# Kernel tuning notes

Hardware: AMD Instinct MI355X
Metric: run time of the kernel (lower is better)

The kernel has to match this reference:

```python
import jax, jax.numpy as jnp
import numpy as np

BS, T = 128, 256
N_AGENTS, STATE_DIM, EMBED_DIM, HYPERNET_EMBED = 32, 512, 64, 256


def setup_inputs() -> dict:
    key = jax.random.key(0)
    ks = jax.random.split(key, 16)
    s = 0.02  # param init scale
    return {
        "agent_qs": jax.random.normal(ks[0], (BS, T, N_AGENTS), jnp.float32),
        "states": jax.random.normal(ks[1], (BS, T, STATE_DIM), jnp.float32),
        "w1_0": jax.random.normal(ks[2], (HYPERNET_EMBED, STATE_DIM), jnp.float32) * s,
        "b1_0": jax.random.normal(ks[3], (HYPERNET_EMBED,), jnp.float32) * s,
        "w1_2": jax.random.normal(ks[4], (EMBED_DIM * N_AGENTS, HYPERNET_EMBED), jnp.float32) * s,
        "b1_2": jax.random.normal(ks[5], (EMBED_DIM * N_AGENTS,), jnp.float32) * s,
        "wf_0": jax.random.normal(ks[6], (HYPERNET_EMBED, STATE_DIM), jnp.float32) * s,
        "bf_0": jax.random.normal(ks[7], (HYPERNET_EMBED,), jnp.float32) * s,
        "wf_2": jax.random.normal(ks[8], (EMBED_DIM, HYPERNET_EMBED), jnp.float32) * s,
        "bf_2": jax.random.normal(ks[9], (EMBED_DIM,), jnp.float32) * s,
        "hb_w": jax.random.normal(ks[10], (EMBED_DIM, STATE_DIM), jnp.float32) * s,
        "hb_b": jax.random.normal(ks[11], (EMBED_DIM,), jnp.float32) * s,
        "v0_w": jax.random.normal(ks[12], (EMBED_DIM, STATE_DIM), jnp.float32) * s,
        "v0_b": jax.random.normal(ks[13], (EMBED_DIM,), jnp.float32) * s,
        "v2_w": jax.random.normal(ks[14], (1, EMBED_DIM), jnp.float32) * s,
        "v2_b": jax.random.normal(ks[15], (1,), jnp.float32) * s,
    }


def reference(agent_qs, states, w1_0, b1_0, w1_2, b1_2, wf_0, bf_0, wf_2, bf_2,
              hb_w, hb_b, v0_w, v0_b, v2_w, v2_b):
    bs = agent_qs.shape[0]
    s = states.reshape(-1, STATE_DIM)          # [B, S]
    q = agent_qs.reshape(-1, 1, N_AGENTS)       # [B, 1, A]
    # hypernet-generated first-layer weights (positive via abs)
    h1 = jax.nn.relu(s @ w1_0.T + b1_0)
    w1 = jnp.abs(h1 @ w1_2.T + b1_2).reshape(-1, N_AGENTS, EMBED_DIM)  # [B, A, E]
    b1 = (s @ hb_w.T + hb_b).reshape(-1, 1, EMBED_DIM)                 # [B, 1, E]
    hidden = jax.nn.elu(jnp.einsum('bia,bae->bie', q, w1) + b1)        # [B, 1, E]
    # hypernet-generated final weights
    hf = jax.nn.relu(s @ wf_0.T + bf_0)
    w_final = jnp.abs(hf @ wf_2.T + bf_2).reshape(-1, EMBED_DIM, 1)    # [B, E, 1]
    v = (jax.nn.relu(s @ v0_w.T + v0_b) @ v2_w.T + v2_b).reshape(-1, 1, 1)
    y = jnp.einsum('bie,beo->bio', hidden, w_final) + v                # [B, 1, 1]
    return y.reshape(bs, -1, 1)
```

## Files before the change

### kernel.cpp

```cpp
#include <hip/hip_runtime.h>


#define SDIM 512
#define HD   256
#define EDIM 64
#define NAG  32

typedef short short8v __attribute__((ext_vector_type(8)));
typedef short short4v __attribute__((ext_vector_type(4)));
typedef float f32x4  __attribute__((ext_vector_type(4)));

__device__ __forceinline__ unsigned short f2bf(float f) {
  unsigned int u = __float_as_uint(f);
  unsigned int r = (u + 0x7FFFu + ((u >> 16) & 1u)) >> 16;
  return (unsigned short)r;
}
__device__ __forceinline__ float bf2f(unsigned short u) {
  return __uint_as_float(((unsigned int)u) << 16);
}
__device__ __forceinline__ short4v cvt4(float4 a) {
  short4v r;
  r[0] = (short)f2bf(a.x); r[1] = (short)f2bf(a.y);
  r[2] = (short)f2bf(a.z); r[3] = (short)f2bf(a.w);
  return r;
}

__global__ void qmix_convert(const float* __restrict__ w1_0, const float* __restrict__ wf_0,
                             const float* __restrict__ hb_w, const float* __restrict__ v0_w,
                             const float* __restrict__ w1_2, const float* __restrict__ wf_2,
                             unsigned short* __restrict__ W0cat, unsigned short* __restrict__ w12b,
                             unsigned short* __restrict__ wf2b) {
  int i = blockIdx.x * 256 + threadIdx.x;
  if (i < 327680) {
    float v;
    if (i < 131072)      v = w1_0[i];
    else if (i < 262144) v = wf_0[i - 131072];
    else if (i < 294912) v = hb_w[i - 262144];
    else                 v = v0_w[i - 294912];
    W0cat[i] = f2bf(v);
  } else if (i < 851968) {
    w12b[i - 327680] = f2bf(w1_2[i - 327680]);
  } else if (i < 868352) {
    wf2b[i - 851968] = f2bf(wf_2[i - 851968]);
  }
}

__global__ __launch_bounds__(512, 1) void qmix_k1(
    const float* __restrict__ states, const unsigned short* __restrict__ W0cat,
    const unsigned short* __restrict__ wf2b,
    const float* __restrict__ b1_0, const float* __restrict__ bf_0,
    const float* __restrict__ hb_b, const float* __restrict__ v0_b,
    const float* __restrict__ v2_w, const float* __restrict__ bf_2,
    unsigned short* __restrict__ h1g, unsigned short* __restrict__ b1h,
    unsigned short* __restrict__ wfinh, float* __restrict__ vbuf)
{
  __shared__ unsigned short sA[128 * 512];

  const int t    = threadIdx.x;
  const int r0   = blockIdx.x * 128;
  const int wave = t >> 6, lane = t & 63;
  const int lrow = lane & 15, lk = lane >> 4;

  const int colbase = wave * 80;
  const unsigned short* bp[5];
#pragma unroll
  for (int f = 0; f < 5; f++)
    bp[f] = W0cat + (size_t)(colbase + f * 16 + lrow) * SDIM + 8 * lk;
  short8v bregs[2][5];
#pragma unroll
  for (int f = 0; f < 5; f++) bregs[0][f] = *(const short8v*)(bp[f]);
#pragma unroll
  for (int f = 0; f < 5; f++) bregs[1][f] = *(const short8v*)(bp[f] + 32);

  const float4* gS4 = (const float4*)(states + (size_t)r0 * SDIM);
  {
    float4 L[16];
#pragma unroll
    for (int h = 0; h < 2; h++) {
#pragma unroll
      for (int it = 0; it < 16; it++) L[it] = gS4[(h * 16 + it) * 512 + t];
#pragma unroll
      for (int it = 0; it < 16; it++) {
        int idx = (h * 16 + it) * 512 + t;
        int row = idx >> 7, c4 = idx & 127;
        int byte = row * 1024 + ((c4 * 8) ^ ((row & 7) << 4));
        *(short4v*)((char*)sA + byte) = cvt4(L[it]);
      }
    }
  }
  __syncthreads();

  f32x4 acc[8][5];
#pragma unroll
  for (int i = 0; i < 8; i++)
#pragma unroll
    for (int f = 0; f < 5; f++) acc[i][f] = (f32x4){0.f, 0.f, 0.f, 0.f};

#pragma unroll 1
  for (int ks = 0; ks < 16; ks++) {
    const int p = ks & 1;
#pragma unroll
    for (int i = 0; i < 8; i++) {
      int row = i * 16 + lrow;
      int byte = row * 1024 + ((ks * 64 + lk * 16) ^ ((row & 7) << 4));
      short8v af = *(const short8v*)((const char*)sA + byte);
#pragma unroll
      for (int f = 0; f < 5; f++)
        acc[i][f] = __builtin_amdgcn_mfma_f32_16x16x32_bf16(af, bregs[p][f], acc[i][f], 0, 0, 0);
    }
    if (ks < 14) {
#pragma unroll
      for (int f = 0; f < 5; f++) bregs[p][f] = *(const short8v*)(bp[f] + (ks + 2) * 32);
    }
  }

  __syncthreads();

  {
    float vs[8][4];
#pragma unroll
    for (int i = 0; i < 8; i++)
#pragma unroll
      for (int rr = 0; rr < 4; rr++) vs[i][rr] = 0.f;

#pragma unroll
    for (int f = 0; f < 5; f++) {
      int cb  = colbase + f * 16;
      int col = cb + lrow;
      if (cb < 512) {
        float bv = (cb < 256) ? b1_0[col] : bf_0[col - 256];
#pragma unroll
        for (int i = 0; i < 8; i++)
#pragma unroll
          for (int rr = 0; rr < 4; rr++) {
            int row = i * 16 + lk * 4 + rr;
            float v = fmaxf(acc[i][f][rr] + bv, 0.f);
            int byte = row * 1024 + ((col * 2) ^ ((row & 7) << 4));
            *(unsigned short*)((char*)sA + byte) = f2bf(v);
          }
      } else if (cb < 576) {
        int e = col - 512;
        float bv = hb_b[e];
#pragma unroll
        for (int i = 0; i < 8; i++)
#pragma unroll
          for (int rr = 0; rr < 4; rr++) {
            int row = i * 16 + lk * 4 + rr;
            b1h[(size_t)(r0 + row) * EDIM + e] = f2bf(acc[i][f][rr] + bv);
          }
      } else {
        int e = col - 576;
        float bv = v0_b[e], wv = v2_w[e];
#pragma unroll
        for (int i = 0; i < 8; i++)
#pragma unroll
          for (int rr = 0; rr < 4; rr++)
            vs[i][rr] = fmaf(fmaxf(acc[i][f][rr] + bv, 0.f), wv, vs[i][rr]);
      }
    }
    if (colbase == 560) {
#pragma unroll
      for (int i = 0; i < 8; i++)
#pragma unroll
        for (int rr = 0; rr < 4; rr++) {
          float v = vs[i][rr];
#pragma unroll
          for (int m = 1; m < 16; m <<= 1) v += __shfl_xor(v, m, 64);
          if (lrow == 0) vbuf[r0 + i * 16 + lk * 4 + rr] = v;
        }
    }
  }
  __syncthreads();

  {
    const int wr2 = wave >> 1;
    const int wc2 = wave & 1;
    f32x4 wfa[2][2];
#pragma unroll
    for (int i2 = 0; i2 < 2; i2++)
#pragma unroll
      for (int j = 0; j < 2; j++) wfa[i2][j] = (f32x4){0.f, 0.f, 0.f, 0.f};
#pragma unroll
    for (int kf = 0; kf < 8; kf++) {
      short8v bf2v[2];
#pragma unroll
      for (int j = 0; j < 2; j++)
        bf2v[j] = *(const short8v*)(wf2b + (size_t)(wc2 * 32 + j * 16 + lrow) * HD + kf * 32 + 8 * lk);
#pragma unroll
      for (int i2 = 0; i2 < 2; i2++) {
        int row = wr2 * 32 + i2 * 16 + lrow;
        int byte = row * 1024 + 512 + ((kf * 64 + lk * 16) ^ ((row & 7) << 4));
        short8v af2 = *(const short8v*)((const char*)sA + byte);
#pragma unroll
        for (int j = 0; j < 2; j++)
          wfa[i2][j] = __builtin_amdgcn_mfma_f32_16x16x32_bf16(af2, bf2v[j], wfa[i2][j], 0, 0, 0);
      }
    }
#pragma unroll
    for (int i2 = 0; i2 < 2; i2++)
#pragma unroll
      for (int j = 0; j < 2; j++) {
        int e = wc2 * 32 + j * 16 + lrow;
#pragma unroll
        for (int r = 0; r < 4; r++) {
          int row = wr2 * 32 + i2 * 16 + lk * 4 + r;
          wfinh[(size_t)(r0 + row) * EDIM + e] = f2bf(fabsf(wfa[i2][j][r] + bf_2[e]));
        }
      }
  }

  {
    char* dst = (char*)h1g + (size_t)r0 * 512;
#pragma unroll
    for (int u = 0; u < 8; u++) {
      int idx = u * 512 + t;
      int row = idx >> 5;
      int p   = (idx & 31) * 16;
      short8v v = *(const short8v*)((const char*)sA + row * 1024 + p);
      *(short8v*)(dst + row * 512 + p) = v;
    }
  }
}

__global__ __launch_bounds__(512, 1) void qmix_k2(
    const unsigned short* __restrict__ h1g, const unsigned short* __restrict__ w12b,
    const float* __restrict__ agent_qs, const float* __restrict__ b1_2,
    const unsigned short* __restrict__ b1h, const unsigned short* __restrict__ wfinh,
    const float* __restrict__ vbuf, const float* __restrict__ v2_b,
    float* __restrict__ out)
{
  __shared__ unsigned char h1s[128 * 512];
  __shared__ unsigned short bbuf[2][16384];
  __shared__ float q_t[NAG * 136];
  __shared__ float ypart[2][128];

  const int t    = threadIdx.x;
  const int r0   = blockIdx.x * 128;
  const int wave = t >> 6, lane = t & 63;
  const int lrow = lane & 15, lk = lane >> 4;
  const int wr = wave >> 1;
  const int wc = wave & 1;

  short8v Lh[8];
  {
    const char* src = (const char*)h1g + (size_t)r0 * 512;
#pragma unroll
    for (int it = 0; it < 8; it++)
      Lh[it] = *(const short8v*)(src + (it * 512 + t) * 16);
  }
  const float4* gq = (const float4*)(agent_qs + (size_t)r0 * NAG);
  float4 q0 = gq[t], q1 = gq[512 + t];
  short8v sreg[4];
#pragma unroll
  for (int rd = 0; rd < 4; rd++)
    sreg[rd] = *(const short8v*)(w12b + rd * 4096 + t * 8);

  {
#pragma unroll
    for (int it = 0; it < 8; it++)
      *(short8v*)(h1s + (it * 512 + t) * 16) = Lh[it];
    int row0 = t >> 3, a4 = (t & 7) * 4;
    q_t[(a4 + 0) * 136 + row0] = q0.x;
    q_t[(a4 + 1) * 136 + row0] = q0.y;
    q_t[(a4 + 2) * 136 + row0] = q0.z;
    q_t[(a4 + 3) * 136 + row0] = q0.w;
    int row1 = 64 + row0;
    q_t[(a4 + 0) * 136 + row1] = q1.x;
    q_t[(a4 + 1) * 136 + row1] = q1.y;
    q_t[(a4 + 2) * 136 + row1] = q1.z;
    q_t[(a4 + 3) * 136 + row1] = q1.w;
#pragma unroll
    for (int rd = 0; rd < 4; rd++) {
      int Lo = rd * 8192 + t * 16;
      *(short8v*)((char*)bbuf + (Lo ^ (((Lo >> 9) & 7) << 4))) = sreg[rd];
    }
  }
  __syncthreads();

  short8v afr[2][8];
#pragma unroll
  for (int i = 0; i < 2; i++) {
    int row = wr * 32 + i * 16 + lrow;
#pragma unroll
    for (int kf = 0; kf < 8; kf++)
      afr[i][kf] = *(const short8v*)(h1s + row * 512 + ((kf * 64 + lk * 16) ^ ((row & 7) << 4)));
  }

  f32x4 hac00 = (f32x4){0.f,0.f,0.f,0.f}, hac01 = (f32x4){0.f,0.f,0.f,0.f};
  f32x4 hac10 = (f32x4){0.f,0.f,0.f,0.f}, hac11 = (f32x4){0.f,0.f,0.f,0.f};

#pragma unroll 1
  for (int a = 0; a < NAG; a++) {
    if (a < NAG - 1) {
      const unsigned short* p = w12b + (size_t)(a + 1) * 16384;
#pragma unroll
      for (int rd = 0; rd < 4; rd++)
        sreg[rd] = *(const short8v*)(p + rd * 4096 + t * 8);
    }
    const char* rbase = (const char*)bbuf + (a & 1) * 32768;

    f32x4 T00 = (f32x4){0.f,0.f,0.f,0.f}, T01 = (f32x4){0.f,0.f,0.f,0.f};
    f32x4 T10 = (f32x4){0.f,0.f,0.f,0.f}, T11 = (f32x4){0.f,0.f,0.f,0.f};
    const int e0 = wc * 32 + lrow, e1 = e0 + 16;
#pragma unroll
    for (int kf = 0; kf < 8; kf++) {
      short8v b0  = *(const short8v*)(rbase + ((e0 * 512 + kf * 64 + lk * 16) ^ ((e0 & 7) << 4)));
      short8v b1v = *(const short8v*)(rbase + ((e1 * 512 + kf * 64 + lk * 16) ^ ((e1 & 7) << 4)));
      T00 = __builtin_amdgcn_mfma_f32_16x16x32_bf16(afr[0][kf], b0,  T00, 0, 0, 0);
      T10 = __builtin_amdgcn_mfma_f32_16x16x32_bf16(afr[1][kf], b0,  T10, 0, 0, 0);
      T01 = __builtin_amdgcn_mfma_f32_16x16x32_bf16(afr[0][kf], b1v, T01, 0, 0, 0);
      T11 = __builtin_amdgcn_mfma_f32_16x16x32_bf16(afr[1][kf], b1v, T11, 0, 0, 0);
    }
    float bb0 = b1_2[a * EDIM + e0];
    float bb1 = b1_2[a * EDIM + e1];
    float4 qa = *(const float4*)(&q_t[a * 136 + wr * 32 + lk * 4]);
    float4 qb = *(const float4*)(&q_t[a * 136 + wr * 32 + 16 + lk * 4]);
#pragma unroll
    for (int r = 0; r < 4; r++) {
      float qar = (r == 0) ? qa.x : (r == 1) ? qa.y : (r == 2) ? qa.z : qa.w;
      float qbr = (r == 0) ? qb.x : (r == 1) ? qb.y : (r == 2) ? qb.z : qb.w;
      hac00[r] = fmaf(qar, fabsf(T00[r] + bb0), hac00[r]);
      hac01[r] = fmaf(qar, fabsf(T01[r] + bb1), hac01[r]);
      hac10[r] = fmaf(qbr, fabsf(T10[r] + bb0), hac10[r]);
      hac11[r] = fmaf(qbr, fabsf(T11[r] + bb1), hac11[r]);
    }
    if (a < NAG - 1) {
      char* wb = (char*)bbuf + ((a & 1) ^ 1) * 32768;
#pragma unroll
      for (int rd = 0; rd < 4; rd++) {
        int Lo = rd * 8192 + t * 16;
        *(short8v*)(wb + (Lo ^ (((Lo >> 9) & 7) << 4))) = sreg[rd];
      }
    }
    __syncthreads();
  }

  {
    float ys0[4], ys1[4];
    const int e0 = wc * 32 + lrow, e1 = e0 + 16;
#pragma unroll
    for (int r = 0; r < 4; r++) {
      int row0 = wr * 32 + lk * 4 + r;
      int row1 = row0 + 16;
      size_t g0 = (size_t)(r0 + row0) * EDIM;
      size_t g1 = (size_t)(r0 + row1) * EDIM;
      float p00 = hac00[r] + bf2f(b1h[g0 + e0]);
      float p01 = hac01[r] + bf2f(b1h[g0 + e1]);
      float p10 = hac10[r] + bf2f(b1h[g1 + e0]);
      float p11 = hac11[r] + bf2f(b1h[g1 + e1]);
      float h00 = p00 > 0.f ? p00 : expm1f(p00);
      float h01 = p01 > 0.f ? p01 : expm1f(p01);
      float h10 = p10 > 0.f ? p10 : expm1f(p10);
      float h11 = p11 > 0.f ? p11 : expm1f(p11);
      ys0[r] = h00 * bf2f(wfinh[g0 + e0]) + h01 * bf2f(wfinh[g0 + e1]);
      ys1[r] = h10 * bf2f(wfinh[g1 + e0]) + h11 * bf2f(wfinh[g1 + e1]);
    }
#pragma unroll
    for (int m = 1; m < 16; m <<= 1)
#pragma unroll
      for (int r = 0; r < 4; r++) {
        ys0[r] += __shfl_xor(ys0[r], m, 64);
        ys1[r] += __shfl_xor(ys1[r], m, 64);
      }
    if (lrow == 0) {
#pragma unroll
      for (int r = 0; r < 4; r++) {
        ypart[wc][wr * 32 + lk * 4 + r]      = ys0[r];
        ypart[wc][wr * 32 + 16 + lk * 4 + r] = ys1[r];
      }
    }
  }
  __syncthreads();
  if (t < 128) {
    out[r0 + t] = ypart[0][t] + ypart[1][t] + vbuf[r0 + t] + v2_b[0];
  }
}

extern "C" void kernel_launch(void* const* d_in, const int* in_sizes, int n_in,
                              void* d_out, int out_size, void* d_ws, size_t ws_size,
                              hipStream_t stream) {
  const float* agent_qs = (const float*)d_in[0];
  const float* states   = (const float*)d_in[1];
  const float* w1_0 = (const float*)d_in[2];
  const float* b1_0 = (const float*)d_in[3];
  const float* w1_2 = (const float*)d_in[4];
  const float* b1_2 = (const float*)d_in[5];
  const float* wf_0 = (const float*)d_in[6];
  const float* bf_0 = (const float*)d_in[7];
  const float* wf_2 = (const float*)d_in[8];
  const float* bf_2 = (const float*)d_in[9];
  const float* hb_w = (const float*)d_in[10];
  const float* hb_b = (const float*)d_in[11];
  const float* v0_w = (const float*)d_in[12];
  const float* v0_b = (const float*)d_in[13];
  const float* v2_w = (const float*)d_in[14];
  const float* v2_b = (const float*)d_in[15];

  char* ws = (char*)d_ws;
  unsigned short* W0cat = (unsigned short*)ws;
  unsigned short* w12b  = (unsigned short*)(ws + 655360);
  unsigned short* wf2b  = (unsigned short*)(ws + 1703936);
  unsigned short* h1g   = (unsigned short*)(ws + 1736704);
  unsigned short* b1h   = (unsigned short*)(ws + 18513920);
  unsigned short* wfinh = (unsigned short*)(ws + 22708224);
  float*          vbuf  = (float*)(ws + 26902528);

  qmix_convert<<<3392, 256, 0, stream>>>(w1_0, wf_0, hb_w, v0_w, w1_2, wf_2,
                                         W0cat, w12b, wf2b);
  qmix_k1<<<256, 512, 0, stream>>>(states, W0cat, wf2b, b1_0, bf_0, hb_b, v0_b,
                                   v2_w, bf_2, h1g, b1h, wfinh, vbuf);
  qmix_k2<<<256, 512, 0, stream>>>(h1g, w12b, agent_qs, b1_2, b1h, wfinh, vbuf,
                                   v2_b, (float*)d_out);
}
```

Before: 125.9 us.

## Split first-stage GEMM into two 64-row halves to cut accumulator registers

The first kernel now processes its 128-row tile as two 64-row halves. Each half runs the full K loop, the epilogue, the wf_2 GEMM and the h1 copy-out. Per-wave accumulators drop from 8x5 to 4x5 fragments, which lowers register pressure. The cost is reloading the W0cat B fragments from global memory twice and adding extra barriers per block. The wf_2 stage also now loads B fragments inside the inner loop instead of sharing them across two row fragments.

```diff
diff --git a/kernel.cpp b/kernel.cpp
--- a/kernel.cpp
+++ b/kernel.cpp
@@ -66,11 +66,6 @@
 #pragma unroll
   for (int f = 0; f < 5; f++)
     bp[f] = W0cat + (size_t)(colbase + f * 16 + lrow) * SDIM + 8 * lk;
-  short8v bregs[2][5];
-#pragma unroll
-  for (int f = 0; f < 5; f++) bregs[0][f] = *(const short8v*)(bp[f]);
-#pragma unroll
-  for (int f = 0; f < 5; f++) bregs[1][f] = *(const short8v*)(bp[f] + 32);
 
   const float4* gS4 = (const float4*)(states + (size_t)r0 * SDIM);
   {
@@ -90,134 +85,136 @@
   }
   __syncthreads();
 
-  f32x4 acc[8][5];
-#pragma unroll
-  for (int i = 0; i < 8; i++)
-#pragma unroll
-    for (int f = 0; f < 5; f++) acc[i][f] = (f32x4){0.f, 0.f, 0.f, 0.f};
-
 #pragma unroll 1
-  for (int ks = 0; ks < 16; ks++) {
-    const int p = ks & 1;
-#pragma unroll
-    for (int i = 0; i < 8; i++) {
-      int row = i * 16 + lrow;
-      int byte = row * 1024 + ((ks * 64 + lk * 16) ^ ((row & 7) << 4));
-      short8v af = *(const short8v*)((const char*)sA + byte);
-#pragma unroll
-      for (int f = 0; f < 5; f++)
-        acc[i][f] = __builtin_amdgcn_mfma_f32_16x16x32_bf16(af, bregs[p][f], acc[i][f], 0, 0, 0);
-    }
-    if (ks < 14) {
-#pragma unroll
-      for (int f = 0; f < 5; f++) bregs[p][f] = *(const short8v*)(bp[f] + (ks + 2) * 32);
-    }
-  }
-
-  __syncthreads();
-
-  {
-    float vs[8][4];
-#pragma unroll
-    for (int i = 0; i < 8; i++)
-#pragma unroll
-      for (int rr = 0; rr < 4; rr++) vs[i][rr] = 0.f;
-
-#pragma unroll
-    for (int f = 0; f < 5; f++) {
-      int cb  = colbase + f * 16;
-      int col = cb + lrow;
-      if (cb < 512) {
-        float bv = (cb < 256) ? b1_0[col] : bf_0[col - 256];
-#pragma unroll
-        for (int i = 0; i < 8; i++)
+  for (int half = 0; half < 2; half++) {
+    const int rbase = half * 64;
+
+    short8v bregs[2][5];
+#pragma unroll
+    for (int f = 0; f < 5; f++) bregs[0][f] = *(const short8v*)(bp[f]);
+#pragma unroll
+    for (int f = 0; f < 5; f++) bregs[1][f] = *(const short8v*)(bp[f] + 32);
+
+    f32x4 acc[4][5];
+#pragma unroll
+    for (int i = 0; i < 4; i++)
+#pragma unroll
+      for (int f = 0; f < 5; f++) acc[i][f] = (f32x4){0.f, 0.f, 0.f, 0.f};
+
+#pragma unroll 1
+    for (int ks = 0; ks < 16; ks++) {
+      const int p = ks & 1;
+#pragma unroll
+      for (int i = 0; i < 4; i++) {
+        int row = rbase + i * 16 + lrow;
+        int byte = row * 1024 + ((ks * 64 + lk * 16) ^ ((row & 7) << 4));
+        short8v af = *(const short8v*)((const char*)sA + byte);
+#pragma unroll
+        for (int f = 0; f < 5; f++)
+          acc[i][f] = __builtin_amdgcn_mfma_f32_16x16x32_bf16(af, bregs[p][f], acc[i][f], 0, 0, 0);
+      }
+      if (ks < 14) {
+#pragma unroll
+        for (int f = 0; f < 5; f++) bregs[p][f] = *(const short8v*)(bp[f] + (ks + 2) * 32);
+      }
+    }
+
+    __syncthreads();
+
+    {
+      float vs[4][4];
+#pragma unroll
+      for (int i = 0; i < 4; i++)
+#pragma unroll
+        for (int rr = 0; rr < 4; rr++) vs[i][rr] = 0.f;
+
+#pragma unroll
+      for (int f = 0; f < 5; f++) {
+        int cb  = colbase + f * 16;
+        int col = cb + lrow;
+        if (cb < 512) {
+          float bv = (cb < 256) ? b1_0[col] : bf_0[col - 256];
+#pragma unroll
+          for (int i = 0; i < 4; i++)
+#pragma unroll
+            for (int rr = 0; rr < 4; rr++) {
+              int row = rbase + i * 16 + lk * 4 + rr;
+              float v = fmaxf(acc[i][f][rr] + bv, 0.f);
+              int byte = row * 1024 + ((col * 2) ^ ((row & 7) << 4));
+              *(unsigned short*)((char*)sA + byte) = f2bf(v);
+            }
+        } else if (cb < 576) {
+          int e = col - 512;
+          float bv = hb_b[e];
+#pragma unroll
+          for (int i = 0; i < 4; i++)
+#pragma unroll
+            for (int rr = 0; rr < 4; rr++) {
+              int row = rbase + i * 16 + lk * 4 + rr;
+              b1h[(size_t)(r0 + row) * EDIM + e] = f2bf(acc[i][f][rr] + bv);
+            }
+        } else {
+          int e = col - 576;
+          float bv = v0_b[e], wv = v2_w[e];
+#pragma unroll
+          for (int i = 0; i < 4; i++)
+#pragma unroll
+            for (int rr = 0; rr < 4; rr++)
+              vs[i][rr] = fmaf(fmaxf(acc[i][f][rr] + bv, 0.f), wv, vs[i][rr]);
+        }
+      }
+      if (colbase == 560) {
+#pragma unroll
+        for (int i = 0; i < 4; i++)
 #pragma unroll
           for (int rr = 0; rr < 4; rr++) {
-            int row = i * 16 + lk * 4 + rr;
-            float v = fmaxf(acc[i][f][rr] + bv, 0.f);
-            int byte = row * 1024 + ((col * 2) ^ ((row & 7) << 4));
-            *(unsigned short*)((char*)sA + byte) = f2bf(v);
+            float v = vs[i][rr];
+#pragma unroll
+            for (int m = 1; m < 16; m <<= 1) v += __shfl_xor(v, m, 64);
+            if (lrow == 0) vbuf[r0 + rbase + i * 16 + lk * 4 + rr] = v;
           }
-      } else if (cb < 576) {
-        int e = col - 512;
-        float bv = hb_b[e];
-#pragma unroll
-        for (int i = 0; i < 8; i++)
-#pragma unroll
-          for (int rr = 0; rr < 4; rr++) {
-            int row = i * 16 + lk * 4 + rr;
-            b1h[(size_t)(r0 + row) * EDIM + e] = f2bf(acc[i][f][rr] + bv);
-          }
-      } else {
-        int e = col - 576;
-        float bv = v0_b[e], wv = v2_w[e];
-#pragma unroll
-        for (int i = 0; i < 8; i++)
-#pragma unroll
-          for (int rr = 0; rr < 4; rr++)
-            vs[i][rr] = fmaf(fmaxf(acc[i][f][rr] + bv, 0.f), wv, vs[i][rr]);
-      }
-    }
-    if (colbase == 560) {
-#pragma unroll
-      for (int i = 0; i < 8; i++)
-#pragma unroll
-        for (int rr = 0; rr < 4; rr++) {
-          float v = vs[i][rr];
-#pragma unroll
-          for (int m = 1; m < 16; m <<= 1) v += __shfl_xor(v, m, 64);
-          if (lrow == 0) vbuf[r0 + i * 16 + lk * 4 + rr] = v;
-        }
-    }
-  }
-  __syncthreads();
-
-  {
-    const int wr2 = wave >> 1;
-    const int wc2 = wave & 1;
-    f32x4 wfa[2][2];
-#pragma unroll
-    for (int i2 = 0; i2 < 2; i2++)
-#pragma unroll
-      for (int j = 0; j < 2; j++) wfa[i2][j] = (f32x4){0.f, 0.f, 0.f, 0.f};
-#pragma unroll
-    for (int kf = 0; kf < 8; kf++) {
-      short8v bf2v[2];
-#pragma unroll
-      for (int j = 0; j < 2; j++)
-        bf2v[j] = *(const short8v*)(wf2b + (size_t)(wc2 * 32 + j * 16 + lrow) * HD + kf * 32 + 8 * lk);
-#pragma unroll
-      for (int i2 = 0; i2 < 2; i2++) {
-        int row = wr2 * 32 + i2 * 16 + lrow;
+      }
+    }
+    __syncthreads();
+
+    {
+      const int wr2 = wave >> 1;
+      const int wc2 = wave & 1;
+      f32x4 wfa[2];
+      wfa[0] = (f32x4){0.f, 0.f, 0.f, 0.f};
+      wfa[1] = (f32x4){0.f, 0.f, 0.f, 0.f};
+      const int row = rbase + wr2 * 16 + lrow;
+#pragma unroll
+      for (int kf = 0; kf < 8; kf++) {
         int byte = row * 1024 + 512 + ((kf * 64 + lk * 16) ^ ((row & 7) << 4));
         short8v af2 = *(const short8v*)((const char*)sA + byte);
 #pragma unroll
-        for (int j = 0; j < 2; j++)
-          wfa[i2][j] = __builtin_amdgcn_mfma_f32_16x16x32_bf16(af2, bf2v[j], wfa[i2][j], 0, 0, 0);
-      }
-    }
-#pragma unroll
-    for (int i2 = 0; i2 < 2; i2++)
+        for (int j = 0; j < 2; j++) {
+          short8v bf2v = *(const short8v*)(wf2b + (size_t)(wc2 * 32 + j * 16 + lrow) * HD + kf * 32 + 8 * lk);
+          wfa[j] = __builtin_amdgcn_mfma_f32_16x16x32_bf16(af2, bf2v, wfa[j], 0, 0, 0);
+        }
+      }
 #pragma unroll
       for (int j = 0; j < 2; j++) {
         int e = wc2 * 32 + j * 16 + lrow;
 #pragma unroll
         for (int r = 0; r < 4; r++) {
-          int row = wr2 * 32 + i2 * 16 + lk * 4 + r;
-          wfinh[(size_t)(r0 + row) * EDIM + e] = f2bf(fabsf(wfa[i2][j][r] + bf_2[e]));
+          int row2 = rbase + wr2 * 16 + lk * 4 + r;
+          wfinh[(size_t)(r0 + row2) * EDIM + e] = f2bf(fabsf(wfa[j][r] + bf_2[e]));
         }
       }
-  }
-
-  {
-    char* dst = (char*)h1g + (size_t)r0 * 512;
-#pragma unroll
-    for (int u = 0; u < 8; u++) {
-      int idx = u * 512 + t;
-      int row = idx >> 5;
-      int p   = (idx & 31) * 16;
-      short8v v = *(const short8v*)((const char*)sA + row * 1024 + p);
-      *(short8v*)(dst + row * 512 + p) = v;
+    }
+
+    {
+      char* dst = (char*)h1g + (size_t)r0 * 512;
+#pragma unroll
+      for (int u = 0; u < 4; u++) {
+        int idx = u * 512 + t;
+        int row = rbase + (idx >> 5);
+        int p   = (idx & 31) * 16;
+        short8v v = *(const short8v*)((const char*)sA + row * 1024 + p);
+        *(short8v*)(dst + row * 512 + p) = v;
+      }
     }
   }
 }
```

Measured after the change: 173.8 us. 38.0% more time.
